# Optimization experiments

Hardware: AMD Instinct MI355X
Metric: run time of the kernel (lower is better)

## Reference

```python
import jax, jax.numpy as jnp
import numpy as np

DIM = 1024
H = 16
DH = DIM // H
EPS = 1e-5
NEG = -1e38


def _layernorm(x, g, b):
    m = jnp.mean(x, axis=-1, keepdims=True)
    v = jnp.mean((x - m) ** 2, axis=-1, keepdims=True)
    return (x - m) / jnp.sqrt(v + EPS) * g + b


def setup_inputs() -> dict:
    key = jax.random.key(0)
    ks = jax.random.split(key, 12)
    B, Nq, Nk = 4, 1024, 1024
    Q = jax.random.normal(ks[0], (B, Nq, DIM), dtype=jnp.float32)
    K = jax.random.normal(ks[1], (B, Nk, DIM), dtype=jnp.float32)
    V = jax.random.normal(ks[2], (B, Nk, DIM), dtype=jnp.float32)
    mask_Q = jax.random.randint(ks[3], (B, Nq), 0, 2).astype(jnp.bool_)
    mask_K = jax.random.randint(ks[4], (B, Nk), 0, 2).astype(jnp.bool_)
    s = 0.02
    Wq = jax.random.normal(ks[5], (DIM, DIM), dtype=jnp.float32) * s
    Wk = jax.random.normal(ks[6], (DIM, DIM), dtype=jnp.float32) * s
    Wv = jax.random.normal(ks[7], (DIM, DIM), dtype=jnp.float32) * s
    Wo = jax.random.normal(ks[8], (DIM, DIM), dtype=jnp.float32) * s
    ln1_g = jnp.ones((DIM,), jnp.float32); ln1_b = jnp.zeros((DIM,), jnp.float32)
    ln2_g = jnp.ones((DIM,), jnp.float32); ln2_b = jnp.zeros((DIM,), jnp.float32)
    return {"Q": Q, "K": K, "V": V, "Wq": Wq, "Wk": Wk, "Wv": Wv, "Wo": Wo,
            "ln1_g": ln1_g, "ln1_b": ln1_b, "ln2_g": ln2_g, "ln2_b": ln2_b,
            "mask_Q": mask_Q, "mask_K": mask_K}


def reference(Q, K, V, Wq, Wk, Wv, Wo, ln1_g, ln1_b, ln2_g, ln2_b, mask_Q, mask_K):
    B, Nq, _ = Q.shape
    Nk = K.shape[1]
    # zero out padded tokens before projection (mask_tensors)
    Qm = jnp.where(mask_Q[..., None], 0.0, Q)
    Km = jnp.where(mask_K[..., None], 0.0, K)
    Vm = jnp.where(mask_K[..., None], 0.0, V)
    # projections (bias=False); torch Linear stores W as [out, in]
    Qp = Qm @ Wq.T
    Kp = Km @ Wk.T
    Vp = Vm @ Wv.T
    # split heads: [B, N, H, DH]
    Qh = Qp.reshape(B, Nq, H, DH)
    Kh = Kp.reshape(B, Nk, H, DH)
    Vh = Vp.reshape(B, Nk, H, DH)
    # NOTE: original scales by sqrt(dim_V), not sqrt(head_dim)
    scores = jnp.einsum('bqhd,bkhd->bhqk', Qh, Kh) / jnp.sqrt(jnp.float32(DIM))
    pad = mask_Q[:, None, :, None] | mask_K[:, None, None, :]  # [B,1,Nq,Nk]
    A = jax.nn.softmax(jnp.where(pad, NEG, scores), axis=-1)
    A = jnp.where(pad, 0.0, A)  # post-softmax masked_fill (dropout = identity in eval)
    O = jnp.einsum('bhqk,bkhd->bqhd', A, Vh).reshape(B, Nq, DIM)
    mq = mask_Q[..., None]
    # residual uses the PROJECTED Q
    O = Qp + O
    O = jnp.where(mq, 0.0, _layernorm(O, ln1_g, ln1_b))
    # masked fc_o then exact (non-tanh) GELU; gelu(0)=0 so masking commutes
    h = jnp.where(mq, 0.0, O @ Wo.T)
    O = O + jax.nn.gelu(h, approximate=False)
    O = jnp.where(mq, 0.0, _layernorm(O, ln2_g, ln2_b))
    return O
```

## Files before the change

### kernel.cpp

```cpp
#include <hip/hip_runtime.h>

#define NTOK 4096
#define AST 72

typedef _Float16 half4v __attribute__((ext_vector_type(4)));
typedef _Float16 half8 __attribute__((ext_vector_type(8)));
typedef float floatx4 __attribute__((ext_vector_type(4)));

__device__ __forceinline__ half8 cvt8(float4 a, float4 b) {
  half8 h;
  h[0] = (_Float16)a.x; h[1] = (_Float16)a.y; h[2] = (_Float16)a.z; h[3] = (_Float16)a.w;
  h[4] = (_Float16)b.x; h[5] = (_Float16)b.y; h[6] = (_Float16)b.z; h[7] = (_Float16)b.w;
  return h;
}

#if defined(__has_builtin)
#if __has_builtin(__builtin_amdgcn_global_load_lds)
#define HAS_GLL 1
#endif
#endif

#ifdef HAS_GLL
#define STAGE16(gp, lp)                                                        \
  __builtin_amdgcn_global_load_lds(                                           \
      (const __attribute__((address_space(1))) void*)(gp),                     \
      (__attribute__((address_space(3))) void*)(lp), 16, 0, 0)
#else
#define STAGE16(gp, lp)                                                        \
  do { *(half8*)((_Float16*)(lp) + lane * 8) = *(const half8*)(gp); } while (0)
#endif

__device__ __forceinline__ int mask_is_bytes(const int* p) {
  int bad = 0;
#pragma unroll
  for (int i = 0; i < 64; i++) bad |= (((unsigned int)p[i]) > 1u);
  return bad;
}

__global__ __launch_bounds__(256) void cvt_all(
    const float* __restrict__ Q, const float* __restrict__ K, const float* __restrict__ V,
    const float* __restrict__ Wq, const float* __restrict__ Wk, const float* __restrict__ Wv,
    const float* __restrict__ Wo,
    const int* __restrict__ srcQ, const int* __restrict__ srcK,
    _Float16* __restrict__ Xq, _Float16* __restrict__ Xk, _Float16* __restrict__ Xv,
    _Float16* __restrict__ Wqh, _Float16* __restrict__ Wkh, _Float16* __restrict__ Wvh,
    _Float16* __restrict__ Woh,
    int* __restrict__ dstQ, int* __restrict__ dstK)
{
  const int blk = blockIdx.x;
  if (blk >= 8192) {
    const int t = (blk - 8192) * 256 + threadIdx.x;
    const int bq = mask_is_bytes(srcQ);
    const int bk = mask_is_bytes(srcK);
    dstQ[t] = bq ? (int)((const unsigned char*)srcQ)[t] : srcQ[t];
    dstK[t] = bk ? (int)((const unsigned char*)srcK)[t] : srcK[t];
    return;
  }
  const float* src; _Float16* dst; size_t off;
  if      (blk < 2048) { src = Q;  dst = Xq;  off = (size_t)blk * 2048; }
  else if (blk < 4096) { src = K;  dst = Xk;  off = (size_t)(blk - 2048) * 2048; }
  else if (blk < 6144) { src = V;  dst = Xv;  off = (size_t)(blk - 4096) * 2048; }
  else if (blk < 6656) { src = Wq; dst = Wqh; off = (size_t)(blk - 6144) * 2048; }
  else if (blk < 7168) { src = Wk; dst = Wkh; off = (size_t)(blk - 6656) * 2048; }
  else if (blk < 7680) { src = Wv; dst = Wvh; off = (size_t)(blk - 7168) * 2048; }
  else                 { src = Wo; dst = Woh; off = (size_t)(blk - 7680) * 2048; }
  const size_t i = off + (size_t)threadIdx.x * 8;
  const float4 a = *(const float4*)(src + i);
  const float4 b = *(const float4*)(src + i + 4);
  *(half8*)(dst + i) = cvt8(a, b);
}

#define GEMM97_CORE(AH, BH)                                                    \
  __shared__ _Float16 sA[2][128 * 32];                                         \
  __shared__ _Float16 sB[2][128 * 32];                                         \
  const int t = threadIdx.x;                                                   \
  const int bn = blockIdx.y, bm = blockIdx.x;                                  \
  const int lane = t & 63, wv = t >> 6, quad = lane >> 4, l16 = lane & 15;     \
  const int wm = wv & 1, wn = wv >> 1;                                         \
  const int srow = wv * 32 + (lane >> 2);                                      \
  const int scol = (lane & 3) * 8;                                             \
  floatx4 acc[4][4] = {};                                                      \
  const _Float16* gA = AH + (size_t)(bm * 128 + srow) * 1024 + scol;           \
  const _Float16* gB = BH + (size_t)(bn * 128 + srow) * 1024 + scol;           \
  STAGE16(gA,         &sA[0][(wv * 32) * 32]);                                 \
  STAGE16(gA + 16384, &sA[0][(wv * 32 + 16) * 32]);                            \
  STAGE16(gB,         &sB[0][(wv * 32) * 32]);                                 \
  STAGE16(gB + 16384, &sB[0][(wv * 32 + 16) * 32]);                            \
  __syncthreads();                                                             \
  for (int kt = 0; kt < 32; kt++) {                                            \
    const int cur = kt & 1;                                                    \
    if (kt < 31) {                                                             \
      STAGE16(gA + (kt + 1) * 32,         &sA[cur ^ 1][(wv * 32) * 32]);       \
      STAGE16(gA + (kt + 1) * 32 + 16384, &sA[cur ^ 1][(wv * 32 + 16) * 32]);  \
      STAGE16(gB + (kt + 1) * 32,         &sB[cur ^ 1][(wv * 32) * 32]);       \
      STAGE16(gB + (kt + 1) * 32 + 16384, &sB[cur ^ 1][(wv * 32 + 16) * 32]);  \
    }                                                                          \
    half8 af[4], bf[4];                                                        \
    _Pragma("unroll")                                                          \
    for (int s = 0; s < 4; s++)                                                \
      af[s] = *(const half8*)&sA[cur][(wm * 64 + s * 16 + l16) * 32 + quad * 8]; \
    _Pragma("unroll")                                                          \
    for (int u = 0; u < 4; u++)                                                \
      bf[u] = *(const half8*)&sB[cur][(wn * 64 + u * 16 + l16) * 32 + quad * 8]; \
    _Pragma("unroll")                                                          \
    for (int s = 0; s < 4; s++)                                                \
      _Pragma("unroll")                                                        \
      for (int u = 0; u < 4; u++)                                              \
        acc[s][u] = __builtin_amdgcn_mfma_f32_16x16x32_f16(af[s], bf[u],       \
                                                           acc[s][u], 0, 0, 0); \
    __syncthreads();                                                           \
  }

__global__ __launch_bounds__(256) void qkv_gemm(
    const _Float16* __restrict__ Xq, const _Float16* __restrict__ Xk,
    const _Float16* __restrict__ Xv,
    const _Float16* __restrict__ Wqh, const _Float16* __restrict__ Wkh,
    const _Float16* __restrict__ Wvh,
    const int* __restrict__ mQ, const int* __restrict__ mK,
    _Float16* __restrict__ Qh, _Float16* __restrict__ Kh, _Float16* __restrict__ Vh)
{
  const int z = blockIdx.z;
  const _Float16* AH = (z == 0) ? Xq : (z == 1) ? Xk : Xv;
  const _Float16* BH = (z == 0) ? Wqh : (z == 1) ? Wkh : Wvh;
  const int* msk = (z == 0) ? mQ : mK;
  _Float16* out = (z == 0) ? Qh : (z == 1) ? Kh : Vh;
  GEMM97_CORE(AH, BH)
#pragma unroll
  for (int s = 0; s < 4; s++)
#pragma unroll
    for (int rr = 0; rr < 4; rr++) {
      const int row = bm * 128 + wm * 64 + s * 16 + quad * 4 + rr;
      const int m = msk[row];
#pragma unroll
      for (int u = 0; u < 4; u++)
        out[(size_t)row * 1024 + bn * 128 + wn * 64 + u * 16 + l16] =
            m ? (_Float16)0.0f : (_Float16)acc[s][u][rr];
    }
}

__global__ __launch_bounds__(256) void gemm_wo(
    const _Float16* __restrict__ AH, const _Float16* __restrict__ BH,
    const float* __restrict__ X1, float* __restrict__ O2)
{
  __shared__ _Float16 sA[2][128 * 32];
  __shared__ _Float16 sB[2][64 * 32];
  const int t = threadIdx.x;
  const int bn = blockIdx.y, bm = blockIdx.x;
  const int lane = t & 63, wv = t >> 6, quad = lane >> 4, l16 = lane & 15;
  const int srowA = wv * 32 + (lane >> 2);
  const int srowB = wv * 16 + (lane >> 2);
  const int scol = (lane & 3) * 8;
  floatx4 acc[2][4] = {};
  const _Float16* gA = AH + (size_t)(bm * 128 + srowA) * 1024 + scol;
  const _Float16* gB = BH + (size_t)(bn * 64 + srowB) * 1024 + scol;
  STAGE16(gA,         &sA[0][(wv * 32) * 32]);
  STAGE16(gA + 16384, &sA[0][(wv * 32 + 16) * 32]);
  STAGE16(gB,         &sB[0][(wv * 16) * 32]);
  __syncthreads();
  for (int kt = 0; kt < 32; kt++) {
    const int cur = kt & 1;
    if (kt < 31) {
      STAGE16(gA + (kt + 1) * 32,         &sA[cur ^ 1][(wv * 32) * 32]);
      STAGE16(gA + (kt + 1) * 32 + 16384, &sA[cur ^ 1][(wv * 32 + 16) * 32]);
      STAGE16(gB + (kt + 1) * 32,         &sB[cur ^ 1][(wv * 16) * 32]);
    }
    half8 af[2], bf[4];
#pragma unroll
    for (int s = 0; s < 2; s++)
      af[s] = *(const half8*)&sA[cur][(wv * 32 + s * 16 + l16) * 32 + quad * 8];
#pragma unroll
    for (int u = 0; u < 4; u++)
      bf[u] = *(const half8*)&sB[cur][(u * 16 + l16) * 32 + quad * 8];
#pragma unroll
    for (int s = 0; s < 2; s++)
#pragma unroll
      for (int u = 0; u < 4; u++)
        acc[s][u] = __builtin_amdgcn_mfma_f32_16x16x32_f16(af[s], bf[u],
                                                           acc[s][u], 0, 0, 0);
    __syncthreads();
  }
#pragma unroll
  for (int s = 0; s < 2; s++)
#pragma unroll
    for (int rr = 0; rr < 4; rr++) {
      const int row = bm * 128 + wv * 32 + s * 16 + quad * 4 + rr;
#pragma unroll
      for (int u = 0; u < 4; u++) {
        const size_t idx = (size_t)row * 1024 + bn * 64 + u * 16 + l16;
        const float hv = acc[s][u][rr];
        const float ge = 0.5f * hv * (1.0f + erff(hv * 0.70710678118654752f));
        O2[idx] = X1[idx] + ge;
      }
    }
}

__global__ __launch_bounds__(256) void v_transpose(
    const _Float16* __restrict__ Vh, _Float16* __restrict__ Vt)
{
  __shared__ _Float16 sT[64 * AST];
  const int t = threadIdx.x;
  const int kt = blockIdx.x, bh = blockIdx.y;
  const int b = bh >> 4, h = bh & 15;
  const int r = t >> 2, c0 = (t & 3) * 16;
  const _Float16* src = Vh + (size_t)(b * 1024 + kt * 64 + r) * 1024 + h * 64 + c0;
  *(half8*)&sT[r * AST + c0] = *(const half8*)src;
  *(half8*)&sT[r * AST + c0 + 8] = *(const half8*)(src + 8);
  __syncthreads();
  half8 o0, o1;
#pragma unroll
  for (int j = 0; j < 8; j++) o0[j] = sT[(c0 + j) * AST + r];
#pragma unroll
  for (int j = 0; j < 8; j++) o1[j] = sT[(c0 + 8 + j) * AST + r];
  _Float16* dst = Vt + ((size_t)bh * 64 + r) * 1024 + kt * 64 + c0;
  *(half8*)dst = o0;
  *(half8*)(dst + 8) = o1;
}

__global__ __launch_bounds__(256) void attn_mfma3(
    const _Float16* __restrict__ Qh, const _Float16* __restrict__ Kh,
    const _Float16* __restrict__ Vt, const int* __restrict__ maskQ,
    const int* __restrict__ maskK, float* __restrict__ O1)
{
  __shared__ _Float16 sK[64 * AST];
  __shared__ _Float16 sV[64 * AST];
  __shared__ _Float16 sQP[64 * AST];
  __shared__ float bias[1024];

  const int t = threadIdx.x;
  const int qt = blockIdx.x, bh = blockIdx.y;
  const int b = bh >> 4, h = bh & 15;
  const int q0 = qt * 64;
  const size_t base = (size_t)b * 1024;
  const int wv = t >> 6, lane = t & 63, quad = lane >> 4, l16 = lane & 15;
  const int r = t >> 2, c0 = (t & 3) * 16;

  const _Float16* kbase = Kh + (base + r) * 1024 + h * 64 + c0;
  const _Float16* vbase = Vt + ((size_t)bh * 64 + r) * 1024 + c0;
  half8 k0v = *(const half8*)kbase;
  half8 k1v = *(const half8*)(kbase + 8);
  half8 v0v = *(const half8*)vbase;
  half8 v1v = *(const half8*)(vbase + 8);

  for (int i = t; i < 1024; i += 256)
    bias[i] = maskK[b * 1024 + i] ? -1e30f : 0.0f;

  {
    const _Float16* qp = Qh + (base + q0 + r) * 1024 + h * 64 + c0;
    *(half8*)&sQP[r * AST + c0] = *(const half8*)qp;
    *(half8*)&sQP[r * AST + c0 + 8] = *(const half8*)(qp + 8);
  }
  __syncthreads();

  const half8 bq0 = *(const half8*)&sQP[(wv * 16 + l16) * AST + quad * 8];
  const half8 bq1 = *(const half8*)&sQP[(wv * 16 + l16) * AST + 32 + quad * 8];

  float l_i = 0.0f;
  floatx4 acc_o[4] = {};

  const float C2 = 0.0450842200277985f;

  for (int kt = 0; kt < 16; kt++) {
    __syncthreads();
    *(half8*)&sK[r * AST + c0]     = k0v;
    *(half8*)&sK[r * AST + c0 + 8] = k1v;
    *(half8*)&sV[r * AST + c0]     = v0v;
    *(half8*)&sV[r * AST + c0 + 8] = v1v;
    __syncthreads();

    if (kt < 15) {
      const _Float16* kp = kbase + (size_t)(kt + 1) * 64 * 1024;
      const _Float16* vp = vbase + (kt + 1) * 64;
      k0v = *(const half8*)kp;
      k1v = *(const half8*)(kp + 8);
      v0v = *(const half8*)vp;
      v1v = *(const half8*)(vp + 8);
    }

    floatx4 s[4] = {};
    __builtin_amdgcn_s_setprio(1);
#pragma unroll
    for (int mt = 0; mt < 4; mt++) {
      const half8 ak0 = *(const half8*)&sK[(mt * 16 + l16) * AST + quad * 8];
      const half8 ak1 = *(const half8*)&sK[(mt * 16 + l16) * AST + 32 + quad * 8];
      s[mt] = __builtin_amdgcn_mfma_f32_16x16x32_f16(ak0, bq0, s[mt], 0, 0, 0);
      s[mt] = __builtin_amdgcn_mfma_f32_16x16x32_f16(ak1, bq1, s[mt], 0, 0, 0);
    }
    __builtin_amdgcn_s_setprio(0);

    float rsum = 0.0f;
#pragma unroll
    for (int mt = 0; mt < 4; mt++) {
      const float4 b4 = *(const float4*)&bias[kt * 64 + mt * 16 + quad * 4];
      const float p0 = __builtin_amdgcn_exp2f(s[mt][0] * C2 + b4.x);
      const float p1 = __builtin_amdgcn_exp2f(s[mt][1] * C2 + b4.y);
      const float p2 = __builtin_amdgcn_exp2f(s[mt][2] * C2 + b4.z);
      const float p3 = __builtin_amdgcn_exp2f(s[mt][3] * C2 + b4.w);
      s[mt][0] = p0; s[mt][1] = p1; s[mt][2] = p2; s[mt][3] = p3;
      rsum += (p0 + p1) + (p2 + p3);
    }
    rsum += __shfl_xor(rsum, 16);
    rsum += __shfl_xor(rsum, 32);
    l_i += rsum;

#pragma unroll
    for (int mt = 0; mt < 4; mt++) {
      half4v pv;
      pv[0] = (_Float16)s[mt][0]; pv[1] = (_Float16)s[mt][1];
      pv[2] = (_Float16)s[mt][2]; pv[3] = (_Float16)s[mt][3];
      *(half4v*)&sQP[(wv * 16 + l16) * AST + mt * 16 + quad * 4] = pv;
    }

    const half8 ap0 = *(const half8*)&sQP[(wv * 16 + l16) * AST + quad * 8];
    const half8 ap1 = *(const half8*)&sQP[(wv * 16 + l16) * AST + 32 + quad * 8];
    __builtin_amdgcn_s_setprio(1);
#pragma unroll
    for (int nt = 0; nt < 4; nt++) {
      const half8 bv0 = *(const half8*)&sV[(nt * 16 + l16) * AST + quad * 8];
      const half8 bv1 = *(const half8*)&sV[(nt * 16 + l16) * AST + 32 + quad * 8];
      acc_o[nt] = __builtin_amdgcn_mfma_f32_16x16x32_f16(ap0, bv0, acc_o[nt], 0, 0, 0);
      acc_o[nt] = __builtin_amdgcn_mfma_f32_16x16x32_f16(ap1, bv1, acc_o[nt], 0, 0, 0);
    }
    __builtin_amdgcn_s_setprio(0);
  }

  float il[4];
#pragma unroll
  for (int rr = 0; rr < 4; rr++) {
    const float lq = __shfl(l_i, quad * 4 + rr);
    il[rr] = (lq > 0.0f) ? 1.0f / lq : 0.0f;
  }
#pragma unroll
  for (int rr = 0; rr < 4; rr++) {
    const int row = q0 + wv * 16 + quad * 4 + rr;
    const int mq = maskQ[b * 1024 + row];
#pragma unroll
    for (int nt = 0; nt < 4; nt++) {
      const size_t gi = (base + row) * 1024 + h * 64 + nt * 16 + l16;
      O1[gi] = mq ? 0.0f : ((float)Qh[gi] + acc_o[nt][rr] * il[rr]);
    }
  }
}

__device__ __forceinline__ void ln_stats(float4 x, int t, float* mean, float* rinv) {
  float s = x.x + x.y + x.z + x.w;
  float s2 = x.x * x.x + x.y * x.y + x.z * x.z + x.w * x.w;
#pragma unroll
  for (int off = 32; off >= 1; off >>= 1) { s += __shfl_xor(s, off); s2 += __shfl_xor(s2, off); }
  __shared__ float red[8];
  __shared__ float sm[2];
  const int wv = t >> 6, lane = t & 63;
  if (lane == 0) { red[wv] = s; red[4 + wv] = s2; }
  __syncthreads();
  if (t == 0) {
    const float S = red[0] + red[1] + red[2] + red[3];
    const float S2 = red[4] + red[5] + red[6] + red[7];
    const float m = S * (1.0f / 1024.0f);
    const float v = S2 * (1.0f / 1024.0f) - m * m;
    sm[0] = m; sm[1] = rsqrtf(v + 1e-5f);
  }
  __syncthreads();
  *mean = sm[0]; *rinv = sm[1];
}

__global__ __launch_bounds__(256) void ln_f32(
    const float* __restrict__ X, const float* __restrict__ g,
    const float* __restrict__ bta, const int* __restrict__ mask,
    float* __restrict__ out)
{
  const int rr = blockIdx.x, t = threadIdx.x, c = 4 * t;
  const float4 x = *(const float4*)&X[(size_t)rr * 1024 + c];
  float mean, ri;
  ln_stats(x, t, &mean, &ri);
  const int msk = mask[rr];
  const float4 gg = *(const float4*)&g[c];
  const float4 bb = *(const float4*)&bta[c];
  float4 o;
  o.x = msk ? 0.f : (x.x - mean) * ri * gg.x + bb.x;
  o.y = msk ? 0.f : (x.y - mean) * ri * gg.y + bb.y;
  o.z = msk ? 0.f : (x.z - mean) * ri * gg.z + bb.z;
  o.w = msk ? 0.f : (x.w - mean) * ri * gg.w + bb.w;
  *(float4*)&out[(size_t)rr * 1024 + c] = o;
}

__global__ __launch_bounds__(256) void ln_f32h(
    const float* __restrict__ X, const float* __restrict__ g,
    const float* __restrict__ bta, const int* __restrict__ mask,
    float* __restrict__ out, _Float16* __restrict__ outh)
{
  const int rr = blockIdx.x, t = threadIdx.x, c = 4 * t;
  const float4 x = *(const float4*)&X[(size_t)rr * 1024 + c];
  float mean, ri;
  ln_stats(x, t, &mean, &ri);
  const int msk = mask[rr];
  const float4 gg = *(const float4*)&g[c];
  const float4 bb = *(const float4*)&bta[c];
  float4 o;
  o.x = msk ? 0.f : (x.x - mean) * ri * gg.x + bb.x;
  o.y = msk ? 0.f : (x.y - mean) * ri * gg.y + bb.y;
  o.z = msk ? 0.f : (x.z - mean) * ri * gg.z + bb.z;
  o.w = msk ? 0.f : (x.w - mean) * ri * gg.w + bb.w;
  const size_t idx = (size_t)rr * 1024 + c;
  *(float4*)&out[idx] = o;
  half4v hh;
  hh[0] = (_Float16)o.x; hh[1] = (_Float16)o.y;
  hh[2] = (_Float16)o.z; hh[3] = (_Float16)o.w;
  *(half4v*)&outh[idx] = hh;
}

extern "C" void kernel_launch(void* const* d_in, const int* in_sizes, int n_in,
                              void* d_out, int out_size, void* d_ws, size_t ws_size,
                              hipStream_t stream)
{
  const float* Q  = (const float*)d_in[0];
  const float* K  = (const float*)d_in[1];
  const float* V  = (const float*)d_in[2];
  const float* Wq = (const float*)d_in[3];
  const float* Wk = (const float*)d_in[4];
  const float* Wv = (const float*)d_in[5];
  const float* Wo = (const float*)d_in[6];
  const float* g1 = (const float*)d_in[7];
  const float* b1 = (const float*)d_in[8];
  const float* g2 = (const float*)d_in[9];
  const float* b2 = (const float*)d_in[10];
  float* out = (float*)d_out;

  char* base = (char*)d_ws;
  const size_t MB_ = 1024 * 1024;
  _Float16* Xq  = (_Float16*)(base +  0 * MB_);
  _Float16* Xk  = (_Float16*)(base +  8 * MB_);
  _Float16* Xv  = (_Float16*)(base + 16 * MB_);
  _Float16* Wqh = (_Float16*)(base + 24 * MB_);
  _Float16* Wkh = (_Float16*)(base + 26 * MB_);
  _Float16* Wvh = (_Float16*)(base + 28 * MB_);
  _Float16* Woh = (_Float16*)(base + 30 * MB_);
  _Float16* Qh  = (_Float16*)(base + 32 * MB_);
  _Float16* Kh  = (_Float16*)(base + 40 * MB_);
  _Float16* Vh  = (_Float16*)(base + 48 * MB_);
  _Float16* Vt  = (_Float16*)(base + 56 * MB_);
  float*    O1  = (float*)(base + 64 * MB_);
  int*      mQ  = (int*)(base + 80 * MB_);
  int*      mK  = mQ + NTOK;
  float*    X1  = (float*)(base + 0 * MB_);
  _Float16* X1h = (_Float16*)(base + 16 * MB_);
  float*    O2  = (float*)(base + 32 * MB_);

  const dim3 bb(256);
  cvt_all<<<dim3(8208), bb, 0, stream>>>(Q, K, V, Wq, Wk, Wv, Wo,
                                         (const int*)d_in[11], (const int*)d_in[12],
                                         Xq, Xk, Xv, Wqh, Wkh, Wvh, Woh, mQ, mK);
  qkv_gemm<<<dim3(32, 8, 3), bb, 0, stream>>>(Xq, Xk, Xv, Wqh, Wkh, Wvh,
                                              mQ, mK, Qh, Kh, Vh);
  v_transpose<<<dim3(16, 64), bb, 0, stream>>>(Vh, Vt);
  attn_mfma3<<<dim3(16, 64), bb, 0, stream>>>(Qh, Kh, Vt, mQ, mK, O1);
  ln_f32h<<<dim3(4096), bb, 0, stream>>>(O1, g1, b1, mQ, X1, X1h);
  gemm_wo<<<dim3(32, 16), bb, 0, stream>>>(X1h, Woh, X1, O2);
  ln_f32<<<dim3(4096), bb, 0, stream>>>(O2, g2, b2, mQ, out);
}
```

Before: 249.0 us.

## Fuse fp32-to-fp16 activation conversion into GEMM A-operand staging

The QKV and Wo GEMMs now read fp32 activations directly and convert them to fp16 in registers before writing to shared memory, replacing the global_load_lds path for the A operand. This removes the separate conversion pass over Q, K and V (48MB read, 24MB written) and the fp16 copy emitted by the first layernorm, shrinking cvt_all to the weights and masks only. In exchange, each GEMM reads twice the A bytes per tile through registers, adding register pressure and VALU conversion work inside the main loop, and A is re-read as fp32 by every N-block.

```diff
diff --git a/kernel.cpp b/kernel.cpp
--- a/kernel.cpp
+++ b/kernel.cpp
@@ -38,93 +38,103 @@
 }
 
 __global__ __launch_bounds__(256) void cvt_all(
-    const float* __restrict__ Q, const float* __restrict__ K, const float* __restrict__ V,
-    const float* __restrict__ Wq, const float* __restrict__ Wk, const float* __restrict__ Wv,
-    const float* __restrict__ Wo,
+    const float* __restrict__ Wq, const float* __restrict__ Wk,
+    const float* __restrict__ Wv, const float* __restrict__ Wo,
     const int* __restrict__ srcQ, const int* __restrict__ srcK,
-    _Float16* __restrict__ Xq, _Float16* __restrict__ Xk, _Float16* __restrict__ Xv,
-    _Float16* __restrict__ Wqh, _Float16* __restrict__ Wkh, _Float16* __restrict__ Wvh,
-    _Float16* __restrict__ Woh,
+    _Float16* __restrict__ Wqh, _Float16* __restrict__ Wkh,
+    _Float16* __restrict__ Wvh, _Float16* __restrict__ Woh,
     int* __restrict__ dstQ, int* __restrict__ dstK)
 {
   const int blk = blockIdx.x;
-  if (blk >= 8192) {
-    const int t = (blk - 8192) * 256 + threadIdx.x;
+  if (blk >= 2048) {
+    const int t = (blk - 2048) * 256 + threadIdx.x;
     const int bq = mask_is_bytes(srcQ);
     const int bk = mask_is_bytes(srcK);
     dstQ[t] = bq ? (int)((const unsigned char*)srcQ)[t] : srcQ[t];
     dstK[t] = bk ? (int)((const unsigned char*)srcK)[t] : srcK[t];
     return;
   }
-  const float* src; _Float16* dst; size_t off;
-  if      (blk < 2048) { src = Q;  dst = Xq;  off = (size_t)blk * 2048; }
-  else if (blk < 4096) { src = K;  dst = Xk;  off = (size_t)(blk - 2048) * 2048; }
-  else if (blk < 6144) { src = V;  dst = Xv;  off = (size_t)(blk - 4096) * 2048; }
-  else if (blk < 6656) { src = Wq; dst = Wqh; off = (size_t)(blk - 6144) * 2048; }
-  else if (blk < 7168) { src = Wk; dst = Wkh; off = (size_t)(blk - 6656) * 2048; }
-  else if (blk < 7680) { src = Wv; dst = Wvh; off = (size_t)(blk - 7168) * 2048; }
-  else                 { src = Wo; dst = Woh; off = (size_t)(blk - 7680) * 2048; }
-  const size_t i = off + (size_t)threadIdx.x * 8;
+  const float* src; _Float16* dst;
+  const int w = blk >> 9;
+  if      (w == 0) { src = Wq; dst = Wqh; }
+  else if (w == 1) { src = Wk; dst = Wkh; }
+  else if (w == 2) { src = Wv; dst = Wvh; }
+  else             { src = Wo; dst = Woh; }
+  const size_t i = (size_t)(blk & 511) * 2048 + (size_t)threadIdx.x * 8;
   const float4 a = *(const float4*)(src + i);
   const float4 b = *(const float4*)(src + i + 4);
   *(half8*)(dst + i) = cvt8(a, b);
 }
 
-#define GEMM97_CORE(AH, BH)                                                    \
-  __shared__ _Float16 sA[2][128 * 32];                                         \
-  __shared__ _Float16 sB[2][128 * 32];                                         \
-  const int t = threadIdx.x;                                                   \
-  const int bn = blockIdx.y, bm = blockIdx.x;                                  \
-  const int lane = t & 63, wv = t >> 6, quad = lane >> 4, l16 = lane & 15;     \
-  const int wm = wv & 1, wn = wv >> 1;                                         \
-  const int srow = wv * 32 + (lane >> 2);                                      \
-  const int scol = (lane & 3) * 8;                                             \
-  floatx4 acc[4][4] = {};                                                      \
-  const _Float16* gA = AH + (size_t)(bm * 128 + srow) * 1024 + scol;           \
-  const _Float16* gB = BH + (size_t)(bn * 128 + srow) * 1024 + scol;           \
-  STAGE16(gA,         &sA[0][(wv * 32) * 32]);                                 \
-  STAGE16(gA + 16384, &sA[0][(wv * 32 + 16) * 32]);                            \
-  STAGE16(gB,         &sB[0][(wv * 32) * 32]);                                 \
-  STAGE16(gB + 16384, &sB[0][(wv * 32 + 16) * 32]);                            \
-  __syncthreads();                                                             \
-  for (int kt = 0; kt < 32; kt++) {                                            \
-    const int cur = kt & 1;                                                    \
-    if (kt < 31) {                                                             \
-      STAGE16(gA + (kt + 1) * 32,         &sA[cur ^ 1][(wv * 32) * 32]);       \
-      STAGE16(gA + (kt + 1) * 32 + 16384, &sA[cur ^ 1][(wv * 32 + 16) * 32]);  \
-      STAGE16(gB + (kt + 1) * 32,         &sB[cur ^ 1][(wv * 32) * 32]);       \
-      STAGE16(gB + (kt + 1) * 32 + 16384, &sB[cur ^ 1][(wv * 32 + 16) * 32]);  \
-    }                                                                          \
-    half8 af[4], bf[4];                                                        \
-    _Pragma("unroll")                                                          \
-    for (int s = 0; s < 4; s++)                                                \
-      af[s] = *(const half8*)&sA[cur][(wm * 64 + s * 16 + l16) * 32 + quad * 8]; \
-    _Pragma("unroll")                                                          \
-    for (int u = 0; u < 4; u++)                                                \
-      bf[u] = *(const half8*)&sB[cur][(wn * 64 + u * 16 + l16) * 32 + quad * 8]; \
-    _Pragma("unroll")                                                          \
-    for (int s = 0; s < 4; s++)                                                \
-      _Pragma("unroll")                                                        \
-      for (int u = 0; u < 4; u++)                                              \
-        acc[s][u] = __builtin_amdgcn_mfma_f32_16x16x32_f16(af[s], bf[u],       \
-                                                           acc[s][u], 0, 0, 0); \
-    __syncthreads();                                                           \
-  }
-
 __global__ __launch_bounds__(256) void qkv_gemm(
-    const _Float16* __restrict__ Xq, const _Float16* __restrict__ Xk,
-    const _Float16* __restrict__ Xv,
+    const float* __restrict__ Qf, const float* __restrict__ Kf,
+    const float* __restrict__ Vf,
     const _Float16* __restrict__ Wqh, const _Float16* __restrict__ Wkh,
     const _Float16* __restrict__ Wvh,
     const int* __restrict__ mQ, const int* __restrict__ mK,
     _Float16* __restrict__ Qh, _Float16* __restrict__ Kh, _Float16* __restrict__ Vh)
 {
+  __shared__ _Float16 sA[2][128 * 32];
+  __shared__ _Float16 sB[2][128 * 32];
   const int z = blockIdx.z;
-  const _Float16* AH = (z == 0) ? Xq : (z == 1) ? Xk : Xv;
+  const float* AF = (z == 0) ? Qf : (z == 1) ? Kf : Vf;
   const _Float16* BH = (z == 0) ? Wqh : (z == 1) ? Wkh : Wvh;
   const int* msk = (z == 0) ? mQ : mK;
   _Float16* out = (z == 0) ? Qh : (z == 1) ? Kh : Vh;
-  GEMM97_CORE(AH, BH)
+  const int t = threadIdx.x;
+  const int bn = blockIdx.y, bm = blockIdx.x;
+  const int lane = t & 63, wv = t >> 6, quad = lane >> 4, l16 = lane & 15;
+  const int wm = wv & 1, wn = wv >> 1;
+  const int srow = wv * 32 + (lane >> 2);
+  const int scol = (lane & 3) * 8;
+  floatx4 acc[4][4] = {};
+  const float* gA = AF + (size_t)(bm * 128 + srow) * 1024 + scol;
+  const _Float16* gB = BH + (size_t)(bn * 128 + srow) * 1024 + scol;
+  _Float16* const wA0 = &sA[0][srow * 32 + scol];
+  _Float16* const wA1 = &sA[1][srow * 32 + scol];
+  {
+    const float4 a0 = *(const float4*)(gA);
+    const float4 a1 = *(const float4*)(gA + 4);
+    const float4 a2 = *(const float4*)(gA + 16384);
+    const float4 a3 = *(const float4*)(gA + 16388);
+    STAGE16(gB,         &sB[0][(wv * 32) * 32]);
+    STAGE16(gB + 16384, &sB[0][(wv * 32 + 16) * 32]);
+    *(half8*)wA0 = cvt8(a0, a1);
+    *(half8*)(wA0 + 16 * 32) = cvt8(a2, a3);
+  }
+  __syncthreads();
+  for (int kt = 0; kt < 32; kt++) {
+    const int cur = kt & 1;
+    float4 a0, a1, a2, a3;
+    if (kt < 31) {
+      const float* g = gA + (kt + 1) * 32;
+      a0 = *(const float4*)(g);
+      a1 = *(const float4*)(g + 4);
+      a2 = *(const float4*)(g + 16384);
+      a3 = *(const float4*)(g + 16388);
+      STAGE16(gB + (kt + 1) * 32,         &sB[cur ^ 1][(wv * 32) * 32]);
+      STAGE16(gB + (kt + 1) * 32 + 16384, &sB[cur ^ 1][(wv * 32 + 16) * 32]);
+    }
+    half8 af[4], bf[4];
+#pragma unroll
+    for (int s = 0; s < 4; s++)
+      af[s] = *(const half8*)&sA[cur][(wm * 64 + s * 16 + l16) * 32 + quad * 8];
+#pragma unroll
+    for (int u = 0; u < 4; u++)
+      bf[u] = *(const half8*)&sB[cur][(wn * 64 + u * 16 + l16) * 32 + quad * 8];
+#pragma unroll
+    for (int s = 0; s < 4; s++)
+#pragma unroll
+      for (int u = 0; u < 4; u++)
+        acc[s][u] = __builtin_amdgcn_mfma_f32_16x16x32_f16(af[s], bf[u],
+                                                           acc[s][u], 0, 0, 0);
+    if (kt < 31) {
+      _Float16* w = (cur ^ 1) ? wA1 : wA0;
+      *(half8*)w = cvt8(a0, a1);
+      *(half8*)(w + 16 * 32) = cvt8(a2, a3);
+    }
+    __syncthreads();
+  }
 #pragma unroll
   for (int s = 0; s < 4; s++)
 #pragma unroll
@@ -139,8 +149,8 @@
 }
 
 __global__ __launch_bounds__(256) void gemm_wo(
-    const _Float16* __restrict__ AH, const _Float16* __restrict__ BH,
-    const float* __restrict__ X1, float* __restrict__ O2)
+    const float* __restrict__ X1, const _Float16* __restrict__ BH,
+    float* __restrict__ O2)
 {
   __shared__ _Float16 sA[2][128 * 32];
   __shared__ _Float16 sB[2][64 * 32];
@@ -151,18 +161,30 @@
   const int srowB = wv * 16 + (lane >> 2);
   const int scol = (lane & 3) * 8;
   floatx4 acc[2][4] = {};
-  const _Float16* gA = AH + (size_t)(bm * 128 + srowA) * 1024 + scol;
+  const float* gA = X1 + (size_t)(bm * 128 + srowA) * 1024 + scol;
   const _Float16* gB = BH + (size_t)(bn * 64 + srowB) * 1024 + scol;
-  STAGE16(gA,         &sA[0][(wv * 32) * 32]);
-  STAGE16(gA + 16384, &sA[0][(wv * 32 + 16) * 32]);
-  STAGE16(gB,         &sB[0][(wv * 16) * 32]);
+  _Float16* const wA0 = &sA[0][srowA * 32 + scol];
+  _Float16* const wA1 = &sA[1][srowA * 32 + scol];
+  {
+    const float4 a0 = *(const float4*)(gA);
+    const float4 a1 = *(const float4*)(gA + 4);
+    const float4 a2 = *(const float4*)(gA + 16384);
+    const float4 a3 = *(const float4*)(gA + 16388);
+    STAGE16(gB, &sB[0][(wv * 16) * 32]);
+    *(half8*)wA0 = cvt8(a0, a1);
+    *(half8*)(wA0 + 16 * 32) = cvt8(a2, a3);
+  }
   __syncthreads();
   for (int kt = 0; kt < 32; kt++) {
     const int cur = kt & 1;
+    float4 a0, a1, a2, a3;
     if (kt < 31) {
-      STAGE16(gA + (kt + 1) * 32,         &sA[cur ^ 1][(wv * 32) * 32]);
-      STAGE16(gA + (kt + 1) * 32 + 16384, &sA[cur ^ 1][(wv * 32 + 16) * 32]);
-      STAGE16(gB + (kt + 1) * 32,         &sB[cur ^ 1][(wv * 16) * 32]);
+      const float* g = gA + (kt + 1) * 32;
+      a0 = *(const float4*)(g);
+      a1 = *(const float4*)(g + 4);
+      a2 = *(const float4*)(g + 16384);
+      a3 = *(const float4*)(g + 16388);
+      STAGE16(gB + (kt + 1) * 32, &sB[cur ^ 1][(wv * 16) * 32]);
     }
     half8 af[2], bf[4];
 #pragma unroll
@@ -177,6 +199,11 @@
       for (int u = 0; u < 4; u++)
         acc[s][u] = __builtin_amdgcn_mfma_f32_16x16x32_f16(af[s], bf[u],
                                                            acc[s][u], 0, 0, 0);
+    if (kt < 31) {
+      _Float16* w = (cur ^ 1) ? wA1 : wA0;
+      *(half8*)w = cvt8(a0, a1);
+      *(half8*)(w + 16 * 32) = cvt8(a2, a3);
+    }
     __syncthreads();
   }
 #pragma unroll
@@ -382,31 +409,6 @@
   *(float4*)&out[(size_t)rr * 1024 + c] = o;
 }
 
-__global__ __launch_bounds__(256) void ln_f32h(
-    const float* __restrict__ X, const float* __restrict__ g,
-    const float* __restrict__ bta, const int* __restrict__ mask,
-    float* __restrict__ out, _Float16* __restrict__ outh)
-{
-  const int rr = blockIdx.x, t = threadIdx.x, c = 4 * t;
-  const float4 x = *(const float4*)&X[(size_t)rr * 1024 + c];
-  float mean, ri;
-  ln_stats(x, t, &mean, &ri);
-  const int msk = mask[rr];
-  const float4 gg = *(const float4*)&g[c];
-  const float4 bb = *(const float4*)&bta[c];
-  float4 o;
-  o.x = msk ? 0.f : (x.x - mean) * ri * gg.x + bb.x;
-  o.y = msk ? 0.f : (x.y - mean) * ri * gg.y + bb.y;
-  o.z = msk ? 0.f : (x.z - mean) * ri * gg.z + bb.z;
-  o.w = msk ? 0.f : (x.w - mean) * ri * gg.w + bb.w;
-  const size_t idx = (size_t)rr * 1024 + c;
-  *(float4*)&out[idx] = o;
-  half4v hh;
-  hh[0] = (_Float16)o.x; hh[1] = (_Float16)o.y;
-  hh[2] = (_Float16)o.z; hh[3] = (_Float16)o.w;
-  *(half4v*)&outh[idx] = hh;
-}
-
 extern "C" void kernel_launch(void* const* d_in, const int* in_sizes, int n_in,
                               void* d_out, int out_size, void* d_ws, size_t ws_size,
                               hipStream_t stream)
@@ -426,9 +428,7 @@
 
   char* base = (char*)d_ws;
   const size_t MB_ = 1024 * 1024;
-  _Float16* Xq  = (_Float16*)(base +  0 * MB_);
-  _Float16* Xk  = (_Float16*)(base +  8 * MB_);
-  _Float16* Xv  = (_Float16*)(base + 16 * MB_);
+  float*    X1  = (float*)(base +  0 * MB_);
   _Float16* Wqh = (_Float16*)(base + 24 * MB_);
   _Float16* Wkh = (_Float16*)(base + 26 * MB_);
   _Float16* Wvh = (_Float16*)(base + 28 * MB_);
@@ -440,19 +440,17 @@
   float*    O1  = (float*)(base + 64 * MB_);
   int*      mQ  = (int*)(base + 80 * MB_);
   int*      mK  = mQ + NTOK;
-  float*    X1  = (float*)(base + 0 * MB_);
-  _Float16* X1h = (_Float16*)(base + 16 * MB_);
   float*    O2  = (float*)(base + 32 * MB_);
 
   const dim3 bb(256);
-  cvt_all<<<dim3(8208), bb, 0, stream>>>(Q, K, V, Wq, Wk, Wv, Wo,
+  cvt_all<<<dim3(2064), bb, 0, stream>>>(Wq, Wk, Wv, Wo,
                                          (const int*)d_in[11], (const int*)d_in[12],
-                                         Xq, Xk, Xv, Wqh, Wkh, Wvh, Woh, mQ, mK);
-  qkv_gemm<<<dim3(32, 8, 3), bb, 0, stream>>>(Xq, Xk, Xv, Wqh, Wkh, Wvh,
+                                         Wqh, Wkh, Wvh, Woh, mQ, mK);
+  qkv_gemm<<<dim3(32, 8, 3), bb, 0, stream>>>(Q, K, V, Wqh, Wkh, Wvh,
                                               mQ, mK, Qh, Kh, Vh);
   v_transpose<<<dim3(16, 64), bb, 0, stream>>>(Vh, Vt);
   attn_mfma3<<<dim3(16, 64), bb, 0, stream>>>(Qh, Kh, Vt, mQ, mK, O1);
-  ln_f32h<<<dim3(4096), bb, 0, stream>>>(O1, g1, b1, mQ, X1, X1h);
-  gemm_wo<<<dim3(32, 16), bb, 0, stream>>>(X1h, Woh, X1, O2);
+  ln_f32<<<dim3(4096), bb, 0, stream>>>(O1, g1, b1, mQ, X1);
+  gemm_wo<<<dim3(32, 16), bb, 0, stream>>>(X1, Woh, O2);
   ln_f32<<<dim3(4096), bb, 0, stream>>>(O2, g2, b2, mQ, out);
 }
```

Result: slower. 266.4 us (+7.0%).
